# Performance work log

Measured on AMD Instinct MI355X. Metric: run time of the kernel, lower is better.

The kernel has to match this reference:

```python
import jax, jax.numpy as jnp
import numpy as np

ALPHA = 0.5
BATCH = 2097152  # 2**21


def _matchgate(theta, phi1, phi2):
    """Matchgate M(theta, phi1, phi2) per Eq (2); returns [B,4,4] complex64.
    Basis ordering |q_i q_j> = 00,01,10,11 (tensorcircuit c.any convention)."""
    c = jnp.cos(theta / 2).astype(jnp.complex64)
    s = jnp.sin(theta / 2).astype(jnp.complex64)
    phi1c = phi1.astype(jnp.complex64)
    phi2c = phi2.astype(jnp.complex64)
    e_ip1 = jnp.exp(1j * phi1c)
    e_mip1 = jnp.exp(-1j * phi1c)
    e_ip2 = jnp.exp(1j * phi2c)
    e_idiff = jnp.exp(1j * (phi2c - phi1c))
    z = jnp.zeros_like(c)
    one = jnp.ones_like(c)
    row0 = jnp.stack([one, z, z, z], -1)
    row1 = jnp.stack([z, c, -e_ip1 * s, z], -1)
    row2 = jnp.stack([z, e_mip1 * s, e_idiff * c, z], -1)
    row3 = jnp.stack([z, z, z, e_ip2], -1)
    return jnp.stack([row0, row1, row2, row3], -2)  # [B,4,4]


def _pair_state(t_a, t_b, m_theta, m_p1, m_p2):
    """Ry(t_a) x Ry(t_b) on |00>, then matchgate. Returns [B,4] complex64."""
    ca, sa = jnp.cos(t_a / 2), jnp.sin(t_a / 2)  # Ry|0> = (cos, sin)
    cb, sb = jnp.cos(t_b / 2), jnp.sin(t_b / 2)
    psi0 = jnp.stack([ca * cb, ca * sb, sa * cb, sa * sb], -1).astype(jnp.complex64)
    M = _matchgate(m_theta, m_p1, m_p2)
    return jnp.einsum('bij,bj->bi', M, psi0)


def _z_exps(psi):
    """<Z_i>, <Z_j>, <Z_i Z_j> for a 2-qubit pair state [B,4]."""
    p = psi.real ** 2 + psi.imag ** 2  # probabilities over 00,01,10,11
    z_i = p[:, 0] + p[:, 1] - p[:, 2] - p[:, 3]
    z_j = p[:, 0] - p[:, 1] + p[:, 2] - p[:, 3]
    zz = p[:, 0] - p[:, 1] - p[:, 2] + p[:, 3]
    return z_i, z_j, zz


def setup_inputs() -> dict:
    key = jax.random.key(0)
    x = jax.random.normal(key, (BATCH, 10), dtype=jnp.float32)
    return {"x": x}


def reference(x):
    t = ALPHA * jnp.tanh(x)  # [B,10]
    # Circuit factorizes: pair (q0,q1) uses t[0],t[1] + matchgate(t4,t5,t6);
    # pair (q2,q3) uses t[2],t[3] + matchgate(t7,t8,t9). No entanglement across pairs.
    psiA = _pair_state(t[:, 0], t[:, 1], t[:, 4], t[:, 5], t[:, 6])
    psiB = _pair_state(t[:, 2], t[:, 3], t[:, 7], t[:, 8], t[:, 9])
    z0, z1, zz01 = _z_exps(psiA)
    z2, z3, zz23 = _z_exps(psiB)
    # Order matches torch: singles z0..z3, then pairs (0,1),(0,2),(0,3),(1,2),(1,3),(2,3)
    out = jnp.stack(
        [z0, z1, z2, z3, zz01, z0 * z2, z0 * z3, z1 * z2, z1 * z3, zz23], -1)
    return out
```

## Files before the change

### kernel.cpp

```cpp
#include <hip/hip_runtime.h>

#define BLOCK 256

typedef float fvec4 __attribute__((ext_vector_type(4)));

__device__ __forceinline__ float fast_tanh(float x) {
    float e = __expf(2.0f * x);
    return 1.0f - 2.0f * __builtin_amdgcn_rcpf(e + 1.0f);
}

__device__ __forceinline__ void pair_z(float ta, float tb, float th, float phi1, float phi2,
                                       float& zi, float& zj, float& zz) {
    float ca, sa, cb, sb, c, s;
    __sincosf(0.5f * ta, &sa, &ca);
    __sincosf(0.5f * tb, &sb, &cb);
    __sincosf(0.5f * th, &s, &c);
    float cp1 = __cosf(phi1);
    float cp2 = __cosf(phi2);

    float u = ca * sb, v = sa * cb;
    float p0 = ca * cb; p0 *= p0;
    float p3 = sa * sb; p3 *= p3;
    float u2 = u * u, v2 = v * v, c2 = c * c, s2 = s * s;
    float cs2uv = 2.0f * c * s * u * v;
    float p1 = c2 * u2 + s2 * v2 - cs2uv * cp1;
    float p2 = s2 * u2 + c2 * v2 + cs2uv * cp2;

    zi = p0 + p1 - p2 - p3;
    zj = p0 - p1 + p2 - p3;
    zz = p0 - p1 - p2 + p3;
}

__device__ __forceinline__ void row_out(float f0, float f1, float f2, float f3, float f4,
                                        float f5, float f6, float f7, float f8, float f9,
                                        float o[10]) {
    float t0 = 0.5f * fast_tanh(f0);
    float t1 = 0.5f * fast_tanh(f1);
    float t2 = 0.5f * fast_tanh(f2);
    float t3 = 0.5f * fast_tanh(f3);
    float t4 = 0.5f * fast_tanh(f4);
    float t5 = 0.5f * fast_tanh(f5);
    float t6 = 0.5f * fast_tanh(f6);
    float t7 = 0.5f * fast_tanh(f7);
    float t8 = 0.5f * fast_tanh(f8);
    float t9 = 0.5f * fast_tanh(f9);

    float z0, z1, zz01, z2, z3, zz23;
    pair_z(t0, t1, t4, t5, t6, z0, z1, zz01);
    pair_z(t2, t3, t7, t8, t9, z2, z3, zz23);

    o[0] = z0; o[1] = z1; o[2] = z2; o[3] = z3;
    o[4] = zz01; o[5] = z0 * z2; o[6] = z0 * z3;
    o[7] = z1 * z2; o[8] = z1 * z3; o[9] = zz23;
}

__global__ void __launch_bounds__(BLOCK)
qfm_kernel(const float* __restrict__ x, float* __restrict__ out, int npairs) {
    int stride = gridDim.x * blockDim.x;
    for (int p = blockIdx.x * blockDim.x + threadIdx.x; p < npairs; p += stride) {
        const fvec4* xp = reinterpret_cast<const fvec4*>(x + (size_t)p * 20);
        fvec4 a0 = xp[0], a1 = xp[1], a2 = xp[2], a3 = xp[3], a4 = xp[4];

        float oA[10], oB[10];
        row_out(a0.x, a0.y, a0.z, a0.w, a1.x, a1.y, a1.z, a1.w, a2.x, a2.y, oA);
        row_out(a2.z, a2.w, a3.x, a3.y, a3.z, a3.w, a4.x, a4.y, a4.z, a4.w, oB);

        fvec4* op = reinterpret_cast<fvec4*>(out + (size_t)p * 20);
        op[0] = fvec4{oA[0], oA[1], oA[2], oA[3]};
        op[1] = fvec4{oA[4], oA[5], oA[6], oA[7]};
        op[2] = fvec4{oA[8], oA[9], oB[0], oB[1]};
        op[3] = fvec4{oB[2], oB[3], oB[4], oB[5]};
        op[4] = fvec4{oB[6], oB[7], oB[8], oB[9]};
    }
}

__global__ void qfm_tail(const float* __restrict__ x, float* __restrict__ out, int row) {
    if (threadIdx.x == 0 && blockIdx.x == 0) {
        const float* xr = x + (size_t)row * 10;
        float o[10];
        row_out(xr[0], xr[1], xr[2], xr[3], xr[4], xr[5], xr[6], xr[7], xr[8], xr[9], o);
        float* orow = out + (size_t)row * 10;
        #pragma unroll
        for (int i = 0; i < 10; ++i) orow[i] = o[i];
    }
}

extern "C" void kernel_launch(void* const* d_in, const int* in_sizes, int n_in,
                              void* d_out, int out_size, void* d_ws, size_t ws_size,
                              hipStream_t stream) {
    const float* x = (const float*)d_in[0];
    float* out = (float*)d_out;
    int B = in_sizes[0] / 10;
    int npairs = B / 2;
    int blocks = (npairs + BLOCK - 1) / BLOCK;
    if (blocks > 2048) blocks = 2048;
    qfm_kernel<<<blocks, BLOCK, 0, stream>>>(x, out, npairs);
    if (B & 1) qfm_tail<<<1, 64, 0, stream>>>(x, out, B - 1);
}
```

Before: 36.94 us.

## Stage input and output chunks through LDS for fully coalesced global access

Each block now loads a 512-row chunk into shared memory with contiguous float4 loads, computes per-thread from LDS, writes the results back to LDS, and stores them to global memory coalesced with nontemporal stores. Before, each thread read and wrote 80-byte strided segments, which leaves lanes' accesses non-contiguous. The cost is three barriers per chunk and LDS traffic. The tail kernel is generalized to handle any remainder rows in parallel.

```diff
diff --git a/kernel.cpp b/kernel.cpp
--- a/kernel.cpp
+++ b/kernel.cpp
@@ -1,6 +1,8 @@
 #include <hip/hip_runtime.h>
 
 #define BLOCK 256
+#define ROWS_PER_CHUNK 512
+#define CHUNK_FLOATS (ROWS_PER_CHUNK * 10)
 
 typedef float fvec4 __attribute__((ext_vector_type(4)));
 
@@ -31,19 +33,17 @@
     zz = p0 - p1 - p2 + p3;
 }
 
-__device__ __forceinline__ void row_out(float f0, float f1, float f2, float f3, float f4,
-                                        float f5, float f6, float f7, float f8, float f9,
-                                        float o[10]) {
-    float t0 = 0.5f * fast_tanh(f0);
-    float t1 = 0.5f * fast_tanh(f1);
-    float t2 = 0.5f * fast_tanh(f2);
-    float t3 = 0.5f * fast_tanh(f3);
-    float t4 = 0.5f * fast_tanh(f4);
-    float t5 = 0.5f * fast_tanh(f5);
-    float t6 = 0.5f * fast_tanh(f6);
-    float t7 = 0.5f * fast_tanh(f7);
-    float t8 = 0.5f * fast_tanh(f8);
-    float t9 = 0.5f * fast_tanh(f9);
+__device__ __forceinline__ void row_out(const float f[10], float o[10]) {
+    float t0 = 0.5f * fast_tanh(f[0]);
+    float t1 = 0.5f * fast_tanh(f[1]);
+    float t2 = 0.5f * fast_tanh(f[2]);
+    float t3 = 0.5f * fast_tanh(f[3]);
+    float t4 = 0.5f * fast_tanh(f[4]);
+    float t5 = 0.5f * fast_tanh(f[5]);
+    float t6 = 0.5f * fast_tanh(f[6]);
+    float t7 = 0.5f * fast_tanh(f[7]);
+    float t8 = 0.5f * fast_tanh(f[8]);
+    float t9 = 0.5f * fast_tanh(f[9]);
 
     float z0, z1, zz01, z2, z3, zz23;
     pair_z(t0, t1, t4, t5, t6, z0, z1, zz01);
@@ -55,34 +55,60 @@
 }
 
 __global__ void __launch_bounds__(BLOCK)
-qfm_kernel(const float* __restrict__ x, float* __restrict__ out, int npairs) {
-    int stride = gridDim.x * blockDim.x;
-    for (int p = blockIdx.x * blockDim.x + threadIdx.x; p < npairs; p += stride) {
-        const fvec4* xp = reinterpret_cast<const fvec4*>(x + (size_t)p * 20);
-        fvec4 a0 = xp[0], a1 = xp[1], a2 = xp[2], a3 = xp[3], a4 = xp[4];
+qfm_kernel(const float* __restrict__ x, float* __restrict__ out, int nchunks) {
+    __shared__ float lds[CHUNK_FLOATS];
+    const int tid = threadIdx.x;
 
+    for (int chunk = blockIdx.x; chunk < nchunks; chunk += gridDim.x) {
+        const size_t base = (size_t)chunk * CHUNK_FLOATS;
+
+        const fvec4* gin = reinterpret_cast<const fvec4*>(x + base);
+        fvec4* lv = reinterpret_cast<fvec4*>(lds);
+        #pragma unroll
+        for (int r = 0; r < 5; ++r)
+            lv[r * BLOCK + tid] = gin[r * BLOCK + tid];
+        __syncthreads();
+
+        float in[20];
+        const fvec4* lrow = reinterpret_cast<const fvec4*>(lds + tid * 20);
+        #pragma unroll
+        for (int k = 0; k < 5; ++k) {
+            fvec4 v = lrow[k];
+            in[4 * k + 0] = v.x; in[4 * k + 1] = v.y;
+            in[4 * k + 2] = v.z; in[4 * k + 3] = v.w;
+        }
         float oA[10], oB[10];
-        row_out(a0.x, a0.y, a0.z, a0.w, a1.x, a1.y, a1.z, a1.w, a2.x, a2.y, oA);
-        row_out(a2.z, a2.w, a3.x, a3.y, a3.z, a3.w, a4.x, a4.y, a4.z, a4.w, oB);
+        row_out(in, oA);
+        row_out(in + 10, oB);
+        __syncthreads();
 
-        fvec4* op = reinterpret_cast<fvec4*>(out + (size_t)p * 20);
-        op[0] = fvec4{oA[0], oA[1], oA[2], oA[3]};
-        op[1] = fvec4{oA[4], oA[5], oA[6], oA[7]};
-        op[2] = fvec4{oA[8], oA[9], oB[0], oB[1]};
-        op[3] = fvec4{oB[2], oB[3], oB[4], oB[5]};
-        op[4] = fvec4{oB[6], oB[7], oB[8], oB[9]};
+        fvec4* lw = reinterpret_cast<fvec4*>(lds + tid * 20);
+        lw[0] = fvec4{oA[0], oA[1], oA[2], oA[3]};
+        lw[1] = fvec4{oA[4], oA[5], oA[6], oA[7]};
+        lw[2] = fvec4{oA[8], oA[9], oB[0], oB[1]};
+        lw[3] = fvec4{oB[2], oB[3], oB[4], oB[5]};
+        lw[4] = fvec4{oB[6], oB[7], oB[8], oB[9]};
+        __syncthreads();
+
+        fvec4* gout = reinterpret_cast<fvec4*>(out + base);
+        #pragma unroll
+        for (int r = 0; r < 5; ++r)
+            __builtin_nontemporal_store(lv[r * BLOCK + tid], gout + r * BLOCK + tid);
     }
 }
 
-__global__ void qfm_tail(const float* __restrict__ x, float* __restrict__ out, int row) {
-    if (threadIdx.x == 0 && blockIdx.x == 0) {
-        const float* xr = x + (size_t)row * 10;
-        float o[10];
-        row_out(xr[0], xr[1], xr[2], xr[3], xr[4], xr[5], xr[6], xr[7], xr[8], xr[9], o);
-        float* orow = out + (size_t)row * 10;
-        #pragma unroll
-        for (int i = 0; i < 10; ++i) orow[i] = o[i];
-    }
+__global__ void qfm_tail(const float* __restrict__ x, float* __restrict__ out,
+                         int row0, int B) {
+    int row = row0 + blockIdx.x * blockDim.x + threadIdx.x;
+    if (row >= B) return;
+    const float* xr = x + (size_t)row * 10;
+    float f[10], o[10];
+    #pragma unroll
+    for (int i = 0; i < 10; ++i) f[i] = xr[i];
+    row_out(f, o);
+    float* orow = out + (size_t)row * 10;
+    #pragma unroll
+    for (int i = 0; i < 10; ++i) orow[i] = o[i];
 }
 
 extern "C" void kernel_launch(void* const* d_in, const int* in_sizes, int n_in,
@@ -91,9 +117,14 @@
     const float* x = (const float*)d_in[0];
     float* out = (float*)d_out;
     int B = in_sizes[0] / 10;
-    int npairs = B / 2;
-    int blocks = (npairs + BLOCK - 1) / BLOCK;
-    if (blocks > 2048) blocks = 2048;
-    qfm_kernel<<<blocks, BLOCK, 0, stream>>>(x, out, npairs);
-    if (B & 1) qfm_tail<<<1, 64, 0, stream>>>(x, out, B - 1);
+    int nchunks = B / ROWS_PER_CHUNK;
+    int blocks = nchunks < 2048 ? (nchunks > 0 ? nchunks : 1) : 2048;
+    if (nchunks > 0)
+        qfm_kernel<<<blocks, BLOCK, 0, stream>>>(x, out, nchunks);
+    int done = nchunks * ROWS_PER_CHUNK;
+    int rem = B - done;
+    if (rem > 0) {
+        int tblocks = (rem + BLOCK - 1) / BLOCK;
+        qfm_tail<<<tblocks, BLOCK, 0, stream>>>(x, out, done, B);
+    }
 }
```

New measurement: 30.77 us. 1.2x faster.
